# Kernel optimization log

Measured on AMD Instinct MI355X. Metric: run time of the kernel, lower is better.

Reference implementation:

```python
import jax, jax.numpy as jnp
import numpy as np

N_NODES = 50000
N_EDGES = 640000
IN_DIM = 4
EMBED = 128
OUT_DIM = 1
N_LAYERS = 3


def setup_inputs() -> dict:
    key = jax.random.key(0)
    ks = jax.random.split(key, 12)
    node_feats = jax.random.normal(ks[0], (N_NODES, IN_DIM), dtype=jnp.float32)
    src = jax.random.randint(ks[1], (N_EDGES,), 0, N_NODES, dtype=jnp.int64 if jax.config.x64_enabled else jnp.int32)
    dst = jax.random.randint(ks[2], (N_EDGES,), 0, N_NODES, dtype=jnp.int64 if jax.config.x64_enabled else jnp.int32)
    s = 1.0 / np.sqrt(EMBED)
    W_emb = jax.random.normal(ks[3], (IN_DIM, EMBED), dtype=jnp.float32) * (1.0 / np.sqrt(IN_DIM))
    b_emb = jnp.zeros((EMBED,), dtype=jnp.float32)
    W_g = jax.random.normal(ks[4], (N_LAYERS, EMBED, EMBED), dtype=jnp.float32) * s
    b_g = jnp.zeros((N_LAYERS, EMBED), dtype=jnp.float32)
    W_o1 = jax.random.normal(ks[5], (EMBED, EMBED), dtype=jnp.float32) * s
    b_o1 = jnp.zeros((EMBED,), dtype=jnp.float32)
    W_o2 = jax.random.normal(ks[6], (EMBED, OUT_DIM), dtype=jnp.float32) * s
    b_o2 = jnp.zeros((OUT_DIM,), dtype=jnp.float32)
    return {"node_feats": node_feats, "src": src, "dst": dst,
            "W_emb": W_emb, "b_emb": b_emb, "W_g": W_g, "b_g": b_g,
            "W_o1": W_o1, "b_o1": b_o1, "W_o2": W_o2, "b_o2": b_o2}


def reference(node_feats, src, dst, W_emb, b_emb, W_g, b_g, W_o1, b_o1, W_o2, b_o2):
    n = node_feats.shape[0]
    ones = jnp.ones(src.shape[0], dtype=node_feats.dtype)
    # DGL GraphConv norm='both': symmetric degree normalization, degrees clamped to >=1
    out_deg = jnp.clip(jax.ops.segment_sum(ones, src, num_segments=n), 1.0)
    in_deg = jnp.clip(jax.ops.segment_sum(ones, dst, num_segments=n), 1.0)
    norm_src = (out_deg ** -0.5)[:, None]  # [N,1]
    norm_dst = (in_deg ** -0.5)[:, None]   # [N,1]

    h = node_feats @ W_emb + b_emb  # [N, E]
    for l in range(W_g.shape[0]):
        x = h * norm_src                                        # scale sources
        agg = jax.ops.segment_sum(x[src], dst, num_segments=n)  # SpMM gather/scatter
        h = agg * norm_dst
        h = h @ W_g[l] + b_g[l]
        h = jax.nn.relu(h)
    h = jax.nn.relu(h @ W_o1 + b_o1)
    return h @ W_o2 + b_o2  # [N, out_dim]
```

## Files before the change

### kernel.cpp

```cpp
#include <hip/hip_runtime.h>

#define NN 50000
#define NE 640000
#define SCAN_B 196

typedef short bf16x8 __attribute__((ext_vector_type(8)));
typedef float f32x4 __attribute__((ext_vector_type(4)));

__device__ __forceinline__ unsigned short f2bf(float f) {
  unsigned int u = __float_as_uint(f);
  unsigned int r = (u + 0x7FFFu + ((u >> 16) & 1u)) >> 16;
  return (unsigned short)r;
}
__device__ __forceinline__ float bf2f(unsigned short h) {
  return __uint_as_float(((unsigned int)h) << 16);
}

typedef const __attribute__((address_space(1))) void* gptr_t;
typedef __attribute__((address_space(3))) void* lptr_t;
__device__ __forceinline__ void gload16(const void* g, void* l) {
  __builtin_amdgcn_global_load_lds((gptr_t)g, (lptr_t)l, 16, 0, 0);
}

__global__ __launch_bounds__(256) void k_deg(const int* __restrict__ src,
                                             const int* __restrict__ dst,
                                             int* __restrict__ out_cnt,
                                             int* __restrict__ in_cnt) {
  int e = blockIdx.x * 256 + threadIdx.x;
  if (e < NE) {
    atomicAdd(&out_cnt[src[e]], 1);
    atomicAdd(&in_cnt[dst[e]], 1);
  }
}

__global__ __launch_bounds__(256) void k_norm(const int* __restrict__ out_cnt,
                                              const int* __restrict__ in_cnt,
                                              float* __restrict__ nsrc,
                                              float* __restrict__ ndst) {
  int n = blockIdx.x * 256 + threadIdx.x;
  if (n < NN) {
    nsrc[n] = 1.0f / sqrtf((float)max(out_cnt[n], 1));
    ndst[n] = 1.0f / sqrtf((float)max(in_cnt[n], 1));
  }
}

__global__ __launch_bounds__(256) void k_scan1(const int* __restrict__ cnt,
                                               int* __restrict__ bsum) {
  int t = threadIdx.x, i = blockIdx.x * 256 + t;
  int v = (i < NN) ? cnt[i] : 0;
#pragma unroll
  for (int o = 32; o >= 1; o >>= 1) v += __shfl_down(v, o);
  __shared__ int ws4[4];
  if ((t & 63) == 0) ws4[t >> 6] = v;
  __syncthreads();
  if (t == 0) bsum[blockIdx.x] = ws4[0] + ws4[1] + ws4[2] + ws4[3];
}

__global__ __launch_bounds__(256) void k_scan2(const int* __restrict__ bsum,
                                               int* __restrict__ boff) {
  int t = threadIdx.x, lane = t & 63, w = t >> 6;
  int v = (t < SCAN_B) ? bsum[t] : 0;
  int sc = v;
#pragma unroll
  for (int o = 1; o < 64; o <<= 1) {
    int x = __shfl_up(sc, o);
    if (lane >= o) sc += x;
  }
  __shared__ int wtot[4];
  if (lane == 63) wtot[w] = sc;
  __syncthreads();
  int base = 0;
  for (int i = 0; i < w; ++i) base += wtot[i];
  if (t < SCAN_B) boff[t] = base + sc - v;
}

__global__ __launch_bounds__(256) void k_scan3(const int* __restrict__ cnt,
                                               const int* __restrict__ boff,
                                               int* __restrict__ row_start) {
  int b = blockIdx.x, t = threadIdx.x, lane = t & 63, w = t >> 6;
  int i = b * 256 + t;
  int v = (i < NN) ? cnt[i] : 0;
  int sc = v;
#pragma unroll
  for (int o = 1; o < 64; o <<= 1) {
    int x = __shfl_up(sc, o);
    if (lane >= o) sc += x;
  }
  __shared__ int wtot[4];
  if (lane == 63) wtot[w] = sc;
  __syncthreads();
  int base = boff[b];
  for (int j = 0; j < w; ++j) base += wtot[j];
  if (i < NN) row_start[i] = base + sc - v;
}

__global__ __launch_bounds__(256) void k_fill(const int* __restrict__ src,
                                              const int* __restrict__ dst,
                                              const int* __restrict__ row_start,
                                              int* __restrict__ cursor,
                                              int* __restrict__ col) {
  int e = blockIdx.x * 256 + threadIdx.x;
  if (e < NE) {
    int d = dst[e];
    int pos = atomicAdd(&cursor[d], 1);
    col[row_start[d] + pos] = src[e];
  }
}

__global__ __launch_bounds__(256) void k_prep(const float* __restrict__ Wg,
                                              const float* __restrict__ Wo1,
                                              unsigned short* __restrict__ wt) {
  int idx = blockIdx.x * 256 + threadIdx.x;
  int mat = idx >> 14, rem = idx & 16383;
  int k = rem >> 7, n = rem & 127;
  const float* Wsrc = (mat < 3) ? (Wg + mat * 16384) : Wo1;
  float v = Wsrc[k * 128 + n];
  unsigned short hi = f2bf(v);
  float lo = v - bf2f(hi);
  unsigned short* base = wt + mat * 32768;
  base[n * 128 + k] = hi;
  base[16384 + n * 128 + k] = f2bf(lo);
}

__global__ __launch_bounds__(256) void k_embed(const float* __restrict__ nf,
                                               const float* __restrict__ W,
                                               const float* __restrict__ b,
                                               const float* __restrict__ nsrc,
                                               float* __restrict__ xs) {
  int idx = blockIdx.x * 256 + threadIdx.x;
  int n = idx >> 7, j = idx & 127;
  const float* f = nf + n * 4;
  float acc = b[j];
  acc += f[0] * W[j] + f[1] * W[128 + j] + f[2] * W[256 + j] + f[3] * W[384 + j];
  xs[idx] = acc * nsrc[n];
}

__global__ __launch_bounds__(256) void k_spmm(const float* __restrict__ xs,
                                              unsigned short* __restrict__ ahi,
                                              unsigned short* __restrict__ alo,
                                              const int* __restrict__ col,
                                              const int* __restrict__ row_start,
                                              const int* __restrict__ in_cnt,
                                              const float* __restrict__ ndst) {
  int node = blockIdx.x * 4 + (threadIdx.x >> 6);
  int lane = threadIdx.x & 63;
  int half = lane >> 5;
  int qlane = lane & 31;
  int start = row_start[node];
  int cnt = in_cnt[node];
  float4 acc = make_float4(0.f, 0.f, 0.f, 0.f);
  const float4* X4 = (const float4*)xs;
  for (int base = 0; base < cnt; base += 64) {
    int m = min(cnt - base, 64);
    int ccol = (lane < m) ? col[start + base + lane] : 0;
    int jj = 0;
    for (; jj + 7 < m; jj += 8) {
      int s0 = __shfl(ccol, jj + half);
      int s1 = __shfl(ccol, jj + 2 + half);
      int s2 = __shfl(ccol, jj + 4 + half);
      int s3 = __shfl(ccol, jj + 6 + half);
      float4 v0 = X4[(size_t)s0 * 32 + qlane];
      float4 v1 = X4[(size_t)s1 * 32 + qlane];
      float4 v2 = X4[(size_t)s2 * 32 + qlane];
      float4 v3 = X4[(size_t)s3 * 32 + qlane];
      acc.x += v0.x + v1.x + v2.x + v3.x;
      acc.y += v0.y + v1.y + v2.y + v3.y;
      acc.z += v0.z + v1.z + v2.z + v3.z;
      acc.w += v0.w + v1.w + v2.w + v3.w;
    }
    for (; jj < m; jj += 2) {
      int j = jj + half;
      int s = __shfl(ccol, (j < m) ? j : 0);
      if (j < m) {
        float4 v = X4[(size_t)s * 32 + qlane];
        acc.x += v.x; acc.y += v.y; acc.z += v.z; acc.w += v.w;
      }
    }
  }
  acc.x += __shfl_down(acc.x, 32);
  acc.y += __shfl_down(acc.y, 32);
  acc.z += __shfl_down(acc.z, 32);
  acc.w += __shfl_down(acc.w, 32);
  if (half == 0) {
    float nd = ndst[node];
    float v0 = acc.x * nd, v1 = acc.y * nd, v2 = acc.z * nd, v3 = acc.w * nd;
    ushort4 h, l;
    h.x = f2bf(v0); l.x = f2bf(v0 - bf2f(h.x));
    h.y = f2bf(v1); l.y = f2bf(v1 - bf2f(h.y));
    h.z = f2bf(v2); l.z = f2bf(v2 - bf2f(h.z));
    h.w = f2bf(v3); l.w = f2bf(v3 - bf2f(h.w));
    *(ushort4*)(ahi + (size_t)node * 128 + qlane * 4) = h;
    *(ushort4*)(alo + (size_t)node * 128 + qlane * 4) = l;
  }
}

__global__ __launch_bounds__(256) void k_gemm_mfma(
    const unsigned short* __restrict__ Ahi, const unsigned short* __restrict__ Alo,
    const unsigned short* __restrict__ Wth, const unsigned short* __restrict__ Wtl,
    const float* __restrict__ bias, float* __restrict__ outf,
    unsigned short* __restrict__ outhi, unsigned short* __restrict__ outlo,
    const float* __restrict__ nsrc, int M, int mode) {
  __shared__ unsigned short sm[2 * 64 * 128];
  int tid = threadIdx.x;
  int lane = tid & 63, w = tid >> 6;
  int tile0 = blockIdx.x * 64;

  {
    int slot = lane & 15;
#pragma unroll
    for (int j = 0; j < 4; ++j) {
      int ldsoff = w * 4096 + j * 1024;
      int row = (ldsoff >> 8) + (lane >> 4);
      int grow = tile0 + row;
      if (grow > M - 1) grow = M - 1;
      size_t gsrc = (size_t)grow * 256 + (size_t)(((slot ^ (row & 7)) << 4));
      gload16((const char*)Ahi + gsrc, (char*)sm + ldsoff);
      gload16((const char*)Alo + gsrc, (char*)sm + 16384 + ldsoff);
    }
  }

  bf16x8 bh[2][4], bl[2][4];
  {
    int koff = (lane >> 4) * 8;
#pragma unroll
    for (int cf = 0; cf < 2; ++cf) {
      int n = w * 32 + cf * 16 + (lane & 15);
      const unsigned short* ph = Wth + (size_t)n * 128 + koff;
      const unsigned short* pl = Wtl + (size_t)n * 128 + koff;
#pragma unroll
      for (int kc = 0; kc < 4; ++kc) {
        bh[cf][kc] = *(const bf16x8*)(ph + kc * 32);
        bl[cf][kc] = *(const bf16x8*)(pl + kc * 32);
      }
    }
  }

  f32x4 acc[4][2] = {};
  __syncthreads();

  int r15 = lane & 15, kq = lane >> 4;
  for (int kc = 0; kc < 4; ++kc) {
    bf16x8 ah[4], al[4];
#pragma unroll
    for (int m = 0; m < 4; ++m) {
      int row = m * 16 + r15;
      int boff = row * 256 + ((((kc * 4 + kq) ^ (row & 7))) << 4);
      ah[m] = *(const bf16x8*)((const char*)sm + boff);
      al[m] = *(const bf16x8*)((const char*)sm + 16384 + boff);
    }
#pragma unroll
    for (int m = 0; m < 4; ++m)
#pragma unroll
      for (int cf = 0; cf < 2; ++cf) {
        acc[m][cf] = __builtin_amdgcn_mfma_f32_16x16x32_bf16(ah[m], bh[cf][kc], acc[m][cf], 0, 0, 0);
        acc[m][cf] = __builtin_amdgcn_mfma_f32_16x16x32_bf16(ah[m], bl[cf][kc], acc[m][cf], 0, 0, 0);
        acc[m][cf] = __builtin_amdgcn_mfma_f32_16x16x32_bf16(al[m], bh[cf][kc], acc[m][cf], 0, 0, 0);
      }
  }

#pragma unroll
  for (int cf = 0; cf < 2; ++cf) {
    int colg = w * 32 + cf * 16 + r15;
    float bv = bias[colg];
#pragma unroll
    for (int m = 0; m < 4; ++m) {
#pragma unroll
      for (int i = 0; i < 4; ++i) {
        int gr = tile0 + m * 16 + kq * 4 + i;
        if (gr < M) {
          float v = fmaxf(acc[m][cf][i] + bv, 0.f);
          if (mode == 0) {
            outf[(size_t)gr * 128 + colg] = v * nsrc[gr];
          } else if (mode == 2) {
            outf[(size_t)gr * 128 + colg] = v;
          } else {
            unsigned short h = f2bf(v);
            outhi[(size_t)gr * 128 + colg] = h;
            outlo[(size_t)gr * 128 + colg] = f2bf(v - bf2f(h));
          }
        }
      }
    }
  }
}

__global__ __launch_bounds__(256) void k_final(const float* __restrict__ h,
                                               const float* __restrict__ W_o2,
                                               const float* __restrict__ b_o2,
                                               float* __restrict__ out) {
  int node = blockIdx.x * 4 + (threadIdx.x >> 6);
  int lane = threadIdx.x & 63;
  float2 v = ((const float2*)(h + (size_t)node * 128))[lane];
  float2 w = ((const float2*)W_o2)[lane];
  float d = v.x * w.x + v.y * w.y;
#pragma unroll
  for (int m = 32; m >= 1; m >>= 1) d += __shfl_xor(d, m);
  if (lane == 0) out[node] = d + b_o2[0];
}

extern "C" void kernel_launch(void* const* d_in, const int* in_sizes, int n_in,
                              void* d_out, int out_size, void* d_ws, size_t ws_size,
                              hipStream_t stream) {
  const float* node_feats = (const float*)d_in[0];
  const int* src = (const int*)d_in[1];
  const int* dst = (const int*)d_in[2];
  const float* W_emb = (const float*)d_in[3];
  const float* b_emb = (const float*)d_in[4];
  const float* W_g = (const float*)d_in[5];
  const float* b_g = (const float*)d_in[6];
  const float* W_o1 = (const float*)d_in[7];
  const float* b_o1 = (const float*)d_in[8];
  const float* W_o2 = (const float*)d_in[9];
  const float* b_o2 = (const float*)d_in[10];
  float* out = (float*)d_out;

  char* ws = (char*)d_ws;
  int* out_cnt   = (int*)(ws + 0);
  int* in_cnt    = (int*)(ws + 200704);
  int* cursor    = (int*)(ws + 401408);
  int* row_start = (int*)(ws + 602112);
  float* nsrc    = (float*)(ws + 802816);
  float* ndst    = (float*)(ws + 1003520);
  int* bsum      = (int*)(ws + 1204224);
  int* boff      = (int*)(ws + 1205248);
  int* col       = (int*)(ws + 1206272);
  unsigned short* wt = (unsigned short*)(ws + 3766272);
  float* X       = (float*)(ws + 4028416);
  unsigned short* Xu = (unsigned short*)(ws + 4028416);
  unsigned short* Ahi = (unsigned short*)(ws + 29628416);
  unsigned short* Alo = (unsigned short*)(ws + 42428416);
  float* Hf      = (float*)(ws + 29628416);

  hipMemsetAsync(d_ws, 0, 602112, stream);

  k_deg<<<(NE + 255) / 256, 256, 0, stream>>>(src, dst, out_cnt, in_cnt);
  k_norm<<<(NN + 255) / 256, 256, 0, stream>>>(out_cnt, in_cnt, nsrc, ndst);
  k_scan1<<<SCAN_B, 256, 0, stream>>>(in_cnt, bsum);
  k_scan2<<<1, 256, 0, stream>>>(bsum, boff);
  k_scan3<<<SCAN_B, 256, 0, stream>>>(in_cnt, boff, row_start);
  k_fill<<<(NE + 255) / 256, 256, 0, stream>>>(src, dst, row_start, cursor, col);
  k_prep<<<256, 256, 0, stream>>>(W_g, W_o1, wt);
  k_embed<<<(NN * 128) / 256, 256, 0, stream>>>(node_feats, W_emb, b_emb, nsrc, X);

  int gemm_grid = (NN + 63) / 64;
  for (int l = 0; l < 3; ++l) {
    k_spmm<<<NN / 4, 256, 0, stream>>>(X, Ahi, Alo, col, row_start, in_cnt, ndst);
    unsigned short* wth = wt + l * 32768;
    unsigned short* wtl = wth + 16384;
    if (l < 2) {
      k_gemm_mfma<<<gemm_grid, 256, 0, stream>>>(Ahi, Alo, wth, wtl, b_g + l * 128,
                                                 X, nullptr, nullptr, nsrc, NN, 0);
    } else {
      k_gemm_mfma<<<gemm_grid, 256, 0, stream>>>(Ahi, Alo, wth, wtl, b_g + l * 128,
                                                 nullptr, Xu, Xu + 6400000, nsrc, NN, 1);
    }
  }
  k_gemm_mfma<<<gemm_grid, 256, 0, stream>>>(Xu, Xu + 6400000, wt + 3 * 32768,
                                             wt + 3 * 32768 + 16384, b_o1,
                                             Hf, nullptr, nullptr, nsrc, NN, 2);
  k_final<<<NN / 4, 256, 0, stream>>>(Hf, W_o2, b_o2, out);
}
```

Measured before the change: 419.5 us.

## Fuse output head into GEMM, reuse degree atomics as CSR rank, predicate SpMM tail

The final Wo1 GEMM now applies bias, ReLU and the dot with W_o2 in its epilogue, reducing through shuffles and shared memory. This removes the fp32 hidden-state round trip and the separate k_final launch. The degree kernel records each edge's atomic return value as its rank, so the CSR fill no longer needs a second atomic pass or cursor memset, and the norm computation is folded into scan1. The SpMM inner loop handles the tail with masked FMAs instead of a scalar remainder loop, trading some wasted loads for fewer branches.

Measured after the change: 385.3 us. 8.1% less time.

```diff
diff --git a/kernel.cpp b/kernel.cpp
--- a/kernel.cpp
+++ b/kernel.cpp
@@ -25,33 +25,32 @@
 __global__ __launch_bounds__(256) void k_deg(const int* __restrict__ src,
                                              const int* __restrict__ dst,
                                              int* __restrict__ out_cnt,
-                                             int* __restrict__ in_cnt) {
+                                             int* __restrict__ in_cnt,
+                                             int* __restrict__ rank) {
   int e = blockIdx.x * 256 + threadIdx.x;
   if (e < NE) {
     atomicAdd(&out_cnt[src[e]], 1);
-    atomicAdd(&in_cnt[dst[e]], 1);
-  }
-}
-
-__global__ __launch_bounds__(256) void k_norm(const int* __restrict__ out_cnt,
-                                              const int* __restrict__ in_cnt,
-                                              float* __restrict__ nsrc,
-                                              float* __restrict__ ndst) {
-  int n = blockIdx.x * 256 + threadIdx.x;
-  if (n < NN) {
-    nsrc[n] = 1.0f / sqrtf((float)max(out_cnt[n], 1));
-    ndst[n] = 1.0f / sqrtf((float)max(in_cnt[n], 1));
-  }
-}
-
-__global__ __launch_bounds__(256) void k_scan1(const int* __restrict__ cnt,
+    rank[e] = atomicAdd(&in_cnt[dst[e]], 1);
+  }
+}
+
+__global__ __launch_bounds__(256) void k_scan1(const int* __restrict__ out_cnt,
+                                               const int* __restrict__ in_cnt,
+                                               float* __restrict__ nsrc,
+                                               float* __restrict__ ndst,
                                                int* __restrict__ bsum) {
   int t = threadIdx.x, i = blockIdx.x * 256 + t;
-  int v = (i < NN) ? cnt[i] : 0;
-#pragma unroll
-  for (int o = 32; o >= 1; o >>= 1) v += __shfl_down(v, o);
+  int v = 0;
+  if (i < NN) {
+    v = in_cnt[i];
+    nsrc[i] = 1.0f / sqrtf((float)max(out_cnt[i], 1));
+    ndst[i] = 1.0f / sqrtf((float)max(v, 1));
+  }
+  int s = v;
+#pragma unroll
+  for (int o = 32; o >= 1; o >>= 1) s += __shfl_down(s, o);
   __shared__ int ws4[4];
-  if ((t & 63) == 0) ws4[t >> 6] = v;
+  if ((t & 63) == 0) ws4[t >> 6] = s;
   __syncthreads();
   if (t == 0) bsum[blockIdx.x] = ws4[0] + ws4[1] + ws4[2] + ws4[3];
 }
@@ -97,13 +96,12 @@
 __global__ __launch_bounds__(256) void k_fill(const int* __restrict__ src,
                                               const int* __restrict__ dst,
                                               const int* __restrict__ row_start,
-                                              int* __restrict__ cursor,
+                                              const int* __restrict__ rank,
                                               int* __restrict__ col) {
   int e = blockIdx.x * 256 + threadIdx.x;
   if (e < NE) {
     int d = dst[e];
-    int pos = atomicAdd(&cursor[d], 1);
-    col[row_start[d] + pos] = src[e];
+    col[row_start[d] + rank[e]] = src[e];
   }
 }
 
@@ -145,7 +143,7 @@
   int node = blockIdx.x * 4 + (threadIdx.x >> 6);
   int lane = threadIdx.x & 63;
   int half = lane >> 5;
-  int qlane = lane & 31;
+  int ql = lane & 31;
   int start = row_start[node];
   int cnt = in_cnt[node];
   float4 acc = make_float4(0.f, 0.f, 0.f, 0.f);
@@ -153,28 +151,29 @@
   for (int base = 0; base < cnt; base += 64) {
     int m = min(cnt - base, 64);
     int ccol = (lane < m) ? col[start + base + lane] : 0;
-    int jj = 0;
-    for (; jj + 7 < m; jj += 8) {
-      int s0 = __shfl(ccol, jj + half);
-      int s1 = __shfl(ccol, jj + 2 + half);
-      int s2 = __shfl(ccol, jj + 4 + half);
-      int s3 = __shfl(ccol, jj + 6 + half);
-      float4 v0 = X4[(size_t)s0 * 32 + qlane];
-      float4 v1 = X4[(size_t)s1 * 32 + qlane];
-      float4 v2 = X4[(size_t)s2 * 32 + qlane];
-      float4 v3 = X4[(size_t)s3 * 32 + qlane];
-      acc.x += v0.x + v1.x + v2.x + v3.x;
-      acc.y += v0.y + v1.y + v2.y + v3.y;
-      acc.z += v0.z + v1.z + v2.z + v3.z;
-      acc.w += v0.w + v1.w + v2.w + v3.w;
-    }
-    for (; jj < m; jj += 2) {
-      int j = jj + half;
-      int s = __shfl(ccol, (j < m) ? j : 0);
-      if (j < m) {
-        float4 v = X4[(size_t)s * 32 + qlane];
-        acc.x += v.x; acc.y += v.y; acc.z += v.z; acc.w += v.w;
-      }
+    for (int jj = 0; jj < m; jj += 8) {
+      int i0 = jj + half, i1 = i0 + 2, i2 = i0 + 4, i3 = i0 + 6;
+      int mm = m - 1;
+      int s0 = __shfl(ccol, min(i0, mm));
+      int s1 = __shfl(ccol, min(i1, mm));
+      int s2 = __shfl(ccol, min(i2, mm));
+      int s3 = __shfl(ccol, min(i3, mm));
+      float f0 = (i0 < m) ? 1.f : 0.f;
+      float f1 = (i1 < m) ? 1.f : 0.f;
+      float f2 = (i2 < m) ? 1.f : 0.f;
+      float f3 = (i3 < m) ? 1.f : 0.f;
+      float4 v0 = X4[(size_t)s0 * 32 + ql];
+      float4 v1 = X4[(size_t)s1 * 32 + ql];
+      float4 v2 = X4[(size_t)s2 * 32 + ql];
+      float4 v3 = X4[(size_t)s3 * 32 + ql];
+      acc.x = fmaf(f0, v0.x, acc.x); acc.y = fmaf(f0, v0.y, acc.y);
+      acc.z = fmaf(f0, v0.z, acc.z); acc.w = fmaf(f0, v0.w, acc.w);
+      acc.x = fmaf(f1, v1.x, acc.x); acc.y = fmaf(f1, v1.y, acc.y);
+      acc.z = fmaf(f1, v1.z, acc.z); acc.w = fmaf(f1, v1.w, acc.w);
+      acc.x = fmaf(f2, v2.x, acc.x); acc.y = fmaf(f2, v2.y, acc.y);
+      acc.z = fmaf(f2, v2.z, acc.z); acc.w = fmaf(f2, v2.w, acc.w);
+      acc.x = fmaf(f3, v3.x, acc.x); acc.y = fmaf(f3, v3.y, acc.y);
+      acc.z = fmaf(f3, v3.z, acc.z); acc.w = fmaf(f3, v3.w, acc.w);
     }
   }
   acc.x += __shfl_down(acc.x, 32);
@@ -189,8 +188,8 @@
     h.y = f2bf(v1); l.y = f2bf(v1 - bf2f(h.y));
     h.z = f2bf(v2); l.z = f2bf(v2 - bf2f(h.z));
     h.w = f2bf(v3); l.w = f2bf(v3 - bf2f(h.w));
-    *(ushort4*)(ahi + (size_t)node * 128 + qlane * 4) = h;
-    *(ushort4*)(alo + (size_t)node * 128 + qlane * 4) = l;
+    *(ushort4*)(ahi + (size_t)node * 128 + ql * 4) = h;
+    *(ushort4*)(alo + (size_t)node * 128 + ql * 4) = l;
   }
 }
 
@@ -199,8 +198,10 @@
     const unsigned short* __restrict__ Wth, const unsigned short* __restrict__ Wtl,
     const float* __restrict__ bias, float* __restrict__ outf,
     unsigned short* __restrict__ outhi, unsigned short* __restrict__ outlo,
-    const float* __restrict__ nsrc, int M, int mode) {
+    const float* __restrict__ nsrc, const float* __restrict__ W_o2,
+    const float* __restrict__ b_o2, int M, int mode) {
   __shared__ unsigned short sm[2 * 64 * 128];
+  __shared__ float smred[4][64];
   int tid = threadIdx.x;
   int lane = tid & 63, w = tid >> 6;
   int tile0 = blockIdx.x * 64;
@@ -258,6 +259,33 @@
       }
   }
 
+  if (mode == 3) {
+    float w2v[2], bv2[2];
+#pragma unroll
+    for (int cf = 0; cf < 2; ++cf) {
+      int colg = w * 32 + cf * 16 + r15;
+      w2v[cf] = W_o2[colg];
+      bv2[cf] = bias[colg];
+    }
+#pragma unroll
+    for (int m = 0; m < 4; ++m) {
+#pragma unroll
+      for (int i = 0; i < 4; ++i) {
+        float p = fmaxf(acc[m][0][i] + bv2[0], 0.f) * w2v[0] +
+                  fmaxf(acc[m][1][i] + bv2[1], 0.f) * w2v[1];
+#pragma unroll
+        for (int msk = 1; msk < 16; msk <<= 1) p += __shfl_xor(p, msk);
+        if (r15 == 0) smred[w][m * 16 + kq * 4 + i] = p;
+      }
+    }
+    __syncthreads();
+    if (tid < 64) {
+      int gr = tile0 + tid;
+      if (gr < M)
+        outf[gr] = smred[0][tid] + smred[1][tid] + smred[2][tid] + smred[3][tid] + b_o2[0];
+    }
+    return;
+  }
 #pragma unroll
   for (int cf = 0; cf < 2; ++cf) {
     int colg = w * 32 + cf * 16 + r15;
@@ -271,8 +299,6 @@
           float v = fmaxf(acc[m][cf][i] + bv, 0.f);
           if (mode == 0) {
             outf[(size_t)gr * 128 + colg] = v * nsrc[gr];
-          } else if (mode == 2) {
-            outf[(size_t)gr * 128 + colg] = v;
           } else {
             unsigned short h = f2bf(v);
             outhi[(size_t)gr * 128 + colg] = h;
@@ -282,20 +308,6 @@
       }
     }
   }
-}
-
-__global__ __launch_bounds__(256) void k_final(const float* __restrict__ h,
-                                               const float* __restrict__ W_o2,
-                                               const float* __restrict__ b_o2,
-                                               float* __restrict__ out) {
-  int node = blockIdx.x * 4 + (threadIdx.x >> 6);
-  int lane = threadIdx.x & 63;
-  float2 v = ((const float2*)(h + (size_t)node * 128))[lane];
-  float2 w = ((const float2*)W_o2)[lane];
-  float d = v.x * w.x + v.y * w.y;
-#pragma unroll
-  for (int m = 32; m >= 1; m >>= 1) d += __shfl_xor(d, m);
-  if (lane == 0) out[node] = d + b_o2[0];
 }
 
 extern "C" void kernel_launch(void* const* d_in, const int* in_sizes, int n_in,
@@ -317,28 +329,26 @@
   char* ws = (char*)d_ws;
   int* out_cnt   = (int*)(ws + 0);
   int* in_cnt    = (int*)(ws + 200704);
-  int* cursor    = (int*)(ws + 401408);
-  int* row_start = (int*)(ws + 602112);
-  float* nsrc    = (float*)(ws + 802816);
-  float* ndst    = (float*)(ws + 1003520);
-  int* bsum      = (int*)(ws + 1204224);
-  int* boff      = (int*)(ws + 1205248);
-  int* col       = (int*)(ws + 1206272);
-  unsigned short* wt = (unsigned short*)(ws + 3766272);
-  float* X       = (float*)(ws + 4028416);
-  unsigned short* Xu = (unsigned short*)(ws + 4028416);
-  unsigned short* Ahi = (unsigned short*)(ws + 29628416);
-  unsigned short* Alo = (unsigned short*)(ws + 42428416);
-  float* Hf      = (float*)(ws + 29628416);
-
-  hipMemsetAsync(d_ws, 0, 602112, stream);
-
-  k_deg<<<(NE + 255) / 256, 256, 0, stream>>>(src, dst, out_cnt, in_cnt);
-  k_norm<<<(NN + 255) / 256, 256, 0, stream>>>(out_cnt, in_cnt, nsrc, ndst);
-  k_scan1<<<SCAN_B, 256, 0, stream>>>(in_cnt, bsum);
+  int* row_start = (int*)(ws + 401408);
+  float* nsrc    = (float*)(ws + 602112);
+  float* ndst    = (float*)(ws + 802816);
+  int* bsum      = (int*)(ws + 1003520);
+  int* boff      = (int*)(ws + 1004544);
+  int* col       = (int*)(ws + 1005568);
+  unsigned short* wt = (unsigned short*)(ws + 3565568);
+  float* X       = (float*)(ws + 3827712);
+  unsigned short* Xu = (unsigned short*)(ws + 3827712);
+  int* rank      = (int*)(ws + 3827712);
+  unsigned short* Ahi = (unsigned short*)(ws + 29427712);
+  unsigned short* Alo = (unsigned short*)(ws + 42227712);
+
+  hipMemsetAsync(d_ws, 0, 401408, stream);
+
+  k_deg<<<(NE + 255) / 256, 256, 0, stream>>>(src, dst, out_cnt, in_cnt, rank);
+  k_scan1<<<SCAN_B, 256, 0, stream>>>(out_cnt, in_cnt, nsrc, ndst, bsum);
   k_scan2<<<1, 256, 0, stream>>>(bsum, boff);
   k_scan3<<<SCAN_B, 256, 0, stream>>>(in_cnt, boff, row_start);
-  k_fill<<<(NE + 255) / 256, 256, 0, stream>>>(src, dst, row_start, cursor, col);
+  k_fill<<<(NE + 255) / 256, 256, 0, stream>>>(src, dst, row_start, rank, col);
   k_prep<<<256, 256, 0, stream>>>(W_g, W_o1, wt);
   k_embed<<<(NN * 128) / 256, 256, 0, stream>>>(node_feats, W_emb, b_emb, nsrc, X);
 
@@ -349,14 +359,16 @@
     unsigned short* wtl = wth + 16384;
     if (l < 2) {
       k_gemm_mfma<<<gemm_grid, 256, 0, stream>>>(Ahi, Alo, wth, wtl, b_g + l * 128,
-                                                 X, nullptr, nullptr, nsrc, NN, 0);
+                                                 X, nullptr, nullptr, nsrc,
+                                                 nullptr, nullptr, NN, 0);
     } else {
       k_gemm_mfma<<<gemm_grid, 256, 0, stream>>>(Ahi, Alo, wth, wtl, b_g + l * 128,
-                                                 nullptr, Xu, Xu + 6400000, nsrc, NN, 1);
+                                                 nullptr, Xu, Xu + 6400000, nsrc,
+                                                 nullptr, nullptr, NN, 1);
     }
   }
   k_gemm_mfma<<<gemm_grid, 256, 0, stream>>>(Xu, Xu + 6400000, wt + 3 * 32768,
                                              wt + 3 * 32768 + 16384, b_o1,
-                                             Hf, nullptr, nullptr, nsrc, NN, 2);
-  k_final<<<NN / 4, 256, 0, stream>>>(Hf, W_o2, b_o2, out);
-}
+                                             out, nullptr, nullptr, nsrc,
+                                             W_o2, b_o2, NN, 3);
+}
```
